# Optimization experiments

Hardware: AMD Instinct MI355X
Metric: run time of the kernel (lower is better)

Reference implementation:

```python
import jax, jax.numpy as jnp
import numpy as np

FH = FW = 3  # kernel_size

# LBP bit weights in raster order over the 8 neighbors (center excluded)
_LBP_W = jnp.array([[1., 2., 4.], [8., 0., 16.], [32., 64., 128.]], dtype=jnp.float32)


def setup_inputs() -> dict:
    key = jax.random.key(0)
    x = jax.random.normal(key, (8, 64, 384, 384), dtype=jnp.float32)
    return {"x": x}


def reference(x) -> jnp.ndarray:
    B, C, H, W = x.shape
    OH, OW = H // FH, W // FW
    # unfold into non-overlapping FHxFW windows: [B,C,OH,OW,FH,FW]
    w = x.reshape(B, C, OH, FH, OW, FW).transpose(0, 1, 2, 4, 3, 5)
    # the four 90-degree rotations of every window: [B,C,OH,OW,4,FH,FW]
    rot = jnp.stack([
        w,
        jnp.rot90(w, 1, axes=(-2, -1)),
        jnp.rot90(w, 2, axes=(-2, -1)),
        jnp.rot90(w, 3, axes=(-2, -1)),
    ], axis=-3)
    # min_lpb: local-binary-pattern key per rotation; pick rotation with min key.
    center = w[..., 1, 1]                                   # [B,C,OH,OW] (rotation-invariant)
    bits = (rot >= center[..., None, None, None]).astype(x.dtype)
    key = jnp.sum(bits * _LBP_W, axis=(-2, -1))             # [B,C,OH,OW,4]
    idx = jnp.argmin(key, axis=-1)                          # [B,C,OH,OW]
    sel = jnp.take_along_axis(rot, idx[..., None, None, None], axis=-3)
    sel = jnp.squeeze(sel, axis=-3)                         # [B,C,OH,OW,FH,FW]
    # fold windows back to the image grid
    out = sel.transpose(0, 1, 2, 4, 3, 5).reshape(B, C, H, W)
    return out
```

## Files before the change

kernel.cpp:

```cpp
#include <hip/hip_runtime.h>

struct F3 { float a, b, c; };

__global__ __launch_bounds__(256) void lbp_min_rot_kernel(
    const float* __restrict__ x, float* __restrict__ out, int nwin) {
    int tid = blockIdx.x * blockDim.x + threadIdx.x;
    if (tid >= nwin) return;

    const int rem = tid & 16383;
    const int bc  = tid >> 14;
    const int oi  = rem >> 7;
    const int oj  = rem & 127;
    const long base = ((long)bc * 384 + 3L * oi) * 384 + 3L * oj;

    const float* p = x + base;
    F3 r0 = *(const F3*)(p);
    F3 r1 = *(const F3*)(p + 384);
    F3 r2 = *(const F3*)(p + 768);
    const float w00 = r0.a, w01 = r0.b, w02 = r0.c;
    const float w10 = r1.a, w11 = r1.b, w12 = r1.c;
    const float w20 = r2.a, w21 = r2.b, w22 = r2.c;

    const float c = w11;
    const int b00 = w00 >= c, b01 = w01 >= c, b02 = w02 >= c;
    const int b10 = w10 >= c,                 b12 = w12 >= c;
    const int b20 = w20 >= c, b21 = w21 >= c, b22 = w22 >= c;

    const int k0 = b00*1 + b01*2 + b02*4 + b10*8 + b12*16 + b20*32 + b21*64 + b22*128;
    const int k1 = b02*1 + b12*2 + b22*4 + b01*8 + b21*16 + b00*32 + b10*64 + b20*128;
    const int k2 = b22*1 + b21*2 + b20*4 + b12*8 + b10*16 + b02*32 + b01*64 + b00*128;
    const int k3 = b20*1 + b10*2 + b00*4 + b21*8 + b01*16 + b22*32 + b12*64 + b02*128;

    int idx = 0, km = k0;
    if (k1 < km) { km = k1; idx = 1; }
    if (k2 < km) { km = k2; idx = 2; }
    if (k3 < km) { km = k3; idx = 3; }

#define SEL4(a, b, cc, d) (idx == 0 ? (a) : idx == 1 ? (b) : idx == 2 ? (cc) : (d))
    const float o00 = SEL4(w00, w02, w22, w20);
    const float o01 = SEL4(w01, w12, w21, w10);
    const float o02 = SEL4(w02, w22, w20, w00);
    const float o10 = SEL4(w10, w01, w12, w21);
    const float o12 = SEL4(w12, w21, w10, w01);
    const float o20 = SEL4(w20, w00, w02, w22);
    const float o21 = SEL4(w21, w10, w01, w12);
    const float o22 = SEL4(w22, w20, w00, w02);
#undef SEL4

    float* q = out + base;
    *(F3*)(q)       = F3{o00, o01, o02};
    *(F3*)(q + 384) = F3{o10, w11, o12};
    *(F3*)(q + 768) = F3{o20, o21, o22};
}

extern "C" void kernel_launch(void* const* d_in, const int* in_sizes, int n_in,
                              void* d_out, int out_size, void* d_ws, size_t ws_size,
                              hipStream_t stream) {
    const float* x = (const float*)d_in[0];
    float* out = (float*)d_out;
    const int total = in_sizes[0];
    const int nwin = total / 9;
    const int block = 256;
    const int grid = (nwin + block - 1) / block;
    lbp_min_rot_kernel<<<grid, block, 0, stream>>>(x, out, nwin);
}
```

Baseline: 110.6 us.

## Stage window rows through LDS with coalesced float4 loads and nontemporal stores

Each block now loads two full 3-row strips (2304 floats) into shared memory with coalesced 16-byte vector loads, computes the min-LBP rotation per window from LDS, writes results back into LDS, then streams the tile out with float4 nontemporal stores. This replaces the strided 12-byte per-thread global accesses, which coalesce poorly. It adds two barriers and LDS traffic with stride-3 bank access, and it assumes the total size is a multiple of 2304 and that rows are 384 wide.

After: 97.29 us. 12.0% less time.

```diff
diff --git a/kernel.cpp b/kernel.cpp
--- a/kernel.cpp
+++ b/kernel.cpp
@@ -1,35 +1,37 @@
 #include <hip/hip_runtime.h>
 
-struct F3 { float a, b, c; };
+typedef float vf4 __attribute__((ext_vector_type(4)));
 
-__global__ __launch_bounds__(256) void lbp_min_rot_kernel(
-    const float* __restrict__ x, float* __restrict__ out, int nwin) {
-    int tid = blockIdx.x * blockDim.x + threadIdx.x;
-    if (tid >= nwin) return;
+__global__ __launch_bounds__(256) void lbp_lds(
+    const float* __restrict__ x, float* __restrict__ out) {
+    __shared__ float tile[2304];
 
-    const int rem = tid & 16383;
-    const int bc  = tid >> 14;
-    const int oi  = rem >> 7;
-    const int oj  = rem & 127;
-    const long base = ((long)bc * 384 + 3L * oi) * 384 + 3L * oj;
+    const int t = threadIdx.x;
+    const long base = (long)blockIdx.x * 2304;
 
-    const float* p = x + base;
-    F3 r0 = *(const F3*)(p);
-    F3 r1 = *(const F3*)(p + 384);
-    F3 r2 = *(const F3*)(p + 768);
-    const float w00 = r0.a, w01 = r0.b, w02 = r0.c;
-    const float w10 = r1.a, w11 = r1.b, w12 = r1.c;
-    const float w20 = r2.a, w21 = r2.b, w22 = r2.c;
+    const vf4* pv = (const vf4*)(x + base);
+    vf4* lv = (vf4*)tile;
+    lv[t]       = pv[t];
+    lv[t + 256] = pv[t + 256];
+    if (t < 64) lv[t + 512] = pv[t + 512];
+    __syncthreads();
+
+    const int wr = t >> 7;
+    const int wc = t & 127;
+    float* wp = tile + wr * 3 * 384 + wc * 3;
+    const float w00 = wp[0],   w01 = wp[1],   w02 = wp[2];
+    const float w10 = wp[384], w11 = wp[385], w12 = wp[386];
+    const float w20 = wp[768], w21 = wp[769], w22 = wp[770];
 
     const float c = w11;
     const int b00 = w00 >= c, b01 = w01 >= c, b02 = w02 >= c;
     const int b10 = w10 >= c,                 b12 = w12 >= c;
     const int b20 = w20 >= c, b21 = w21 >= c, b22 = w22 >= c;
 
-    const int k0 = b00*1 + b01*2 + b02*4 + b10*8 + b12*16 + b20*32 + b21*64 + b22*128;
-    const int k1 = b02*1 + b12*2 + b22*4 + b01*8 + b21*16 + b00*32 + b10*64 + b20*128;
-    const int k2 = b22*1 + b21*2 + b20*4 + b12*8 + b10*16 + b02*32 + b01*64 + b00*128;
-    const int k3 = b20*1 + b10*2 + b00*4 + b21*8 + b01*16 + b22*32 + b12*64 + b02*128;
+    const int k0 = b00 + b01*2 + b02*4 + b10*8 + b12*16 + b20*32 + b21*64 + b22*128;
+    const int k1 = b02 + b12*2 + b22*4 + b01*8 + b21*16 + b00*32 + b10*64 + b20*128;
+    const int k2 = b22 + b21*2 + b20*4 + b12*8 + b10*16 + b02*32 + b01*64 + b00*128;
+    const int k3 = b20 + b10*2 + b00*4 + b21*8 + b01*16 + b22*32 + b12*64 + b02*128;
 
     int idx = 0, km = k0;
     if (k1 < km) { km = k1; idx = 1; }
@@ -37,20 +39,22 @@
     if (k3 < km) { km = k3; idx = 3; }
 
 #define SEL4(a, b, cc, d) (idx == 0 ? (a) : idx == 1 ? (b) : idx == 2 ? (cc) : (d))
-    const float o00 = SEL4(w00, w02, w22, w20);
-    const float o01 = SEL4(w01, w12, w21, w10);
-    const float o02 = SEL4(w02, w22, w20, w00);
-    const float o10 = SEL4(w10, w01, w12, w21);
-    const float o12 = SEL4(w12, w21, w10, w01);
-    const float o20 = SEL4(w20, w00, w02, w22);
-    const float o21 = SEL4(w21, w10, w01, w12);
-    const float o22 = SEL4(w22, w20, w00, w02);
+    wp[0]   = SEL4(w00, w02, w22, w20);
+    wp[1]   = SEL4(w01, w12, w21, w10);
+    wp[2]   = SEL4(w02, w22, w20, w00);
+    wp[384] = SEL4(w10, w01, w12, w21);
+    wp[386] = SEL4(w12, w21, w10, w01);
+    wp[768] = SEL4(w20, w00, w02, w22);
+    wp[769] = SEL4(w21, w10, w01, w12);
+    wp[770] = SEL4(w22, w20, w00, w02);
 #undef SEL4
 
-    float* q = out + base;
-    *(F3*)(q)       = F3{o00, o01, o02};
-    *(F3*)(q + 384) = F3{o10, w11, o12};
-    *(F3*)(q + 768) = F3{o20, o21, o22};
+    __syncthreads();
+
+    vf4* qv = (vf4*)(out + base);
+    __builtin_nontemporal_store(lv[t], qv + t);
+    __builtin_nontemporal_store(lv[t + 256], qv + t + 256);
+    if (t < 64) __builtin_nontemporal_store(lv[t + 512], qv + t + 512);
 }
 
 extern "C" void kernel_launch(void* const* d_in, const int* in_sizes, int n_in,
@@ -59,8 +63,6 @@
     const float* x = (const float*)d_in[0];
     float* out = (float*)d_out;
     const int total = in_sizes[0];
-    const int nwin = total / 9;
-    const int block = 256;
-    const int grid = (nwin + block - 1) / block;
-    lbp_min_rot_kernel<<<grid, block, 0, stream>>>(x, out, nwin);
+    const int grid = total / 2304;
+    lbp_lds<<<grid, 256, 0, stream>>>(x, out);
 }
```
